# Performance work log

Measured on AMD Instinct MI355X. Metric: run time of the kernel, lower is better.

The kernel has to match this reference:

```python
import jax, jax.numpy as jnp
import numpy as np

# Mega (Flash-Quad) encoder layer: MultiHeadEMA + moving-average gated chunked attention + ScaleNorm
L, B, D = 2048, 16, 512        # seq_len, batch, embed_dim (fairseq L,B,D layout)
H, Z, NDIM = 1024, 128, 2      # hdim, zdim, EMA ndim
CHUNK = 128                    # Flash-Quad chunk size
MAXPOS = 1024                  # SimpleRelativePositionalBias max positions
EPS = 1e-6                     # ScaleNorm eps


def setup_inputs() -> dict:
    key = jax.random.key(0)
    ks = jax.random.split(key, 16)
    def nrm(k, shape, s=0.02):
        return jax.random.normal(k, shape, jnp.float32) * s
    return dict(
        x=jax.random.normal(ks[0], (L, B, D), jnp.float32),
        # MultiHeadEMA params (bidirectional -> kernel_dim = 2*D)
        ema_delta=nrm(ks[1], (2 * D, NDIM, 1), 1.0),
        ema_alpha=nrm(ks[2], (2 * D, NDIM, 1), 1.0),
        ema_beta=nrm(ks[3], (2 * D, NDIM, 1), 0.02),
        ema_gamma=nrm(ks[4], (2 * D, NDIM), 1.0),
        ema_omega=nrm(ks[5], (D,), 1.0),
        # projections
        Wv=nrm(ks[6], (D, H)), bv=jnp.zeros((H,), jnp.float32),
        Wmx=nrm(ks[7], (D, Z + H + 2 * D)), bmx=jnp.zeros((Z + H + 2 * D,), jnp.float32),
        Wh=nrm(ks[8], (H, D)), bh=jnp.zeros((D,), jnp.float32),
        # per-dim q/k affine (gamma/beta) on shared z
        qk_gamma=nrm(ks[9], (2, Z), 0.1) + 1.0,
        qk_beta=nrm(ks[10], (2, Z), 0.1),
        # simple relative positional bias over chunk length
        rel_pos_bias=nrm(ks[11], (2 * MAXPOS - 1,), 0.02),
        # ScaleNorm scalar
        norm_scalar=jnp.ones((), jnp.float32),
    )


def _ema(x, delta, alpha, beta, gamma, omega):
    """Bidirectional multi-dim damped EMA via FFT convolution. x: (L,B,D) -> (L,B,D)."""
    Lx, Bx, Dx = x.shape
    residual = x * omega
    xt = jnp.transpose(x, (1, 2, 0))                      # B,D,L
    p = jax.nn.sigmoid(delta)                             # 2D,n,1
    q = 1.0 - p * jax.nn.sigmoid(alpha)                   # 2D,n,1 in (0,1)
    vander = jnp.arange(Lx, dtype=jnp.float32)[None, None, :] * jnp.log(q)  # 2D,n,L
    kern = jnp.einsum('dnl,dn->dl', (p * beta) * jnp.exp(vander),
                      gamma * (1.0 / np.sqrt(NDIM)))      # 2D,L
    k1, k2 = kern[:Dx], kern[Dx:]
    # combined causal + anticausal kernel of length 2L-1, input left-padded by L-1
    kc = jnp.pad(k1, ((0, 0), (Lx - 1, 0))) + jnp.pad(k2[:, ::-1], ((0, 0), (0, Lx - 1)))
    xp = jnp.pad(xt, ((0, 0), (0, 0), (Lx - 1, 0)))
    n = 2 * (2 * Lx - 1)
    out = jnp.fft.irfft(jnp.fft.rfft(xp, n=n) * jnp.fft.rfft(kc, n=n), n=n)
    out = out[..., 2 * Lx - 2: 2 * Lx - 2 + Lx]           # B,D,L
    return jax.nn.silu(jnp.transpose(out, (2, 0, 1)) + residual)


def _forward(x, ema_delta, ema_alpha, ema_beta, ema_gamma, ema_omega,
             Wv, bv, Wmx, bmx, Wh, bh, qk_gamma, qk_beta, rel_pos_bias, norm_scalar):
    Lx, Bx, Dx = x.shape
    residual = x
    v = jax.nn.silu(x @ Wv + bv)                          # L,B,H
    mx = _ema(x, ema_delta, ema_alpha, ema_beta, ema_gamma, ema_omega)  # L,B,D
    base = mx @ Wmx + bmx                                 # L,B,D+Z+H+D
    u = jax.nn.sigmoid(base[..., :Dx])                    # update gate
    zr = jax.nn.silu(base[..., Dx:Dx + Z + H])
    hx = base[..., Dx + Z + H:]
    z, r = zr[..., :Z], zr[..., Z:]                       # shared z, reset gate r
    zqk = z[..., None, :] * qk_gamma + qk_beta            # L,B,2,Z
    nc = Lx // CHUNK
    q = jnp.transpose(zqk[..., 0, :], (1, 0, 2)).reshape(Bx, nc, CHUNK, Z)
    k = jnp.transpose(zqk[..., 1, :], (1, 0, 2)).reshape(Bx, nc, CHUNK, Z)
    vc = jnp.transpose(v, (1, 0, 2)).reshape(Bx, nc, CHUNK, H)
    # Toeplitz relative bias: bias[i,j] = rel_pos_bias[MAXPOS-1 + j - i]
    idx = (MAXPOS - 1) + jnp.arange(CHUNK)[None, :] - jnp.arange(CHUNK)[:, None]
    bias = rel_pos_bias[idx]                              # C,C
    qk = jnp.einsum('bnqz,bnkz->bnqk', q * (Z ** -0.5), k) + bias
    attn = jax.nn.softmax(qk, axis=-1)                    # B,nc,C,C
    h = jnp.einsum('bnqk,bnkh->bnqh', attn, vc).reshape(Bx, Lx, H)
    h = jnp.transpose(h, (1, 0, 2))                       # L,B,H
    h = jax.nn.silu(hx + (h * r) @ Wh + bh)               # L,B,D
    out = residual + u * (h - residual)                   # addcmul gated residual
    ms = jnp.mean(out * out, axis=-1, keepdims=True)      # ScaleNorm
    out = norm_scalar * out * jax.lax.rsqrt(ms + EPS)
    return out, attn


def reference(x, ema_delta, ema_alpha, ema_beta, ema_gamma, ema_omega,
              Wv, bv, Wmx, bmx, Wh, bh, qk_gamma, qk_beta, rel_pos_bias, norm_scalar):
    return _forward(x, ema_delta, ema_alpha, ema_beta, ema_gamma, ema_omega,
                    Wv, bv, Wmx, bmx, Wh, bh, qk_gamma, qk_beta, rel_pos_bias, norm_scalar)
```

## Files before the change

### kernel.cpp

```cpp
#include <hip/hip_runtime.h>
#include <math.h>

#define L_DIM 2048
#define B_DIM 16
#define D_DIM 512
#define H_DIM 1024
#define Z_DIM 128
#define NC    16
#define BASE_N 2176
#define ROWS  (L_DIM*B_DIM)
#define NSEG  32
#define SLEN  64
#define CHAINS 8192

typedef unsigned short bf16_t;
typedef __attribute__((ext_vector_type(8))) short short8;
typedef __attribute__((ext_vector_type(4))) float f32x4;

__device__ __forceinline__ float sigmoidf_(float x){ return 1.f/(1.f+__expf(-x)); }
__device__ __forceinline__ float siluf_(float x){ return x/(1.f+__expf(-x)); }
__device__ __forceinline__ float fbits(unsigned int b){ union{unsigned int i; float f;} c; c.i=b; return c.f; }
__device__ __forceinline__ unsigned short f2bf(float f){
  union{float f; unsigned int i;} c; c.f=f;
  unsigned int r = c.i + 0x7FFFu + ((c.i>>16)&1u);
  return (unsigned short)(r>>16);
}
__device__ __forceinline__ float bf2f(unsigned short u){ return fbits(((unsigned int)u)<<16); }

__device__ __forceinline__ void load8(const float* __restrict__ p, float* d){
  float4 a = *(const float4*)p; float4 b = *(const float4*)(p+4);
  d[0]=a.x; d[1]=a.y; d[2]=a.z; d[3]=a.w; d[4]=b.x; d[5]=b.y; d[6]=b.z; d[7]=b.w;
}
__device__ __forceinline__ void load8(const bf16_t* __restrict__ p, float* d){
  uint4 u = *(const uint4*)p;
  d[0]=fbits(u.x<<16); d[1]=fbits(u.x&0xFFFF0000u);
  d[2]=fbits(u.y<<16); d[3]=fbits(u.y&0xFFFF0000u);
  d[4]=fbits(u.z<<16); d[5]=fbits(u.z&0xFFFF0000u);
  d[6]=fbits(u.w<<16); d[7]=fbits(u.w&0xFFFF0000u);
}
__device__ __forceinline__ void store8bf(bf16_t* p, const float* v){
  uint4 s;
  s.x = (unsigned int)f2bf(v[0]) | ((unsigned int)f2bf(v[1])<<16);
  s.y = (unsigned int)f2bf(v[2]) | ((unsigned int)f2bf(v[3])<<16);
  s.z = (unsigned int)f2bf(v[4]) | ((unsigned int)f2bf(v[5])<<16);
  s.w = (unsigned int)f2bf(v[6]) | ((unsigned int)f2bf(v[7])<<16);
  *(uint4*)p = s;
}

__device__ __forceinline__ void glds16(const void* g, void* l) {
  __builtin_amdgcn_global_load_lds(
      (const __attribute__((address_space(1))) unsigned int*)g,
      (__attribute__((address_space(3))) unsigned int*)l, 16, 0, 0);
}

__global__ __launch_bounds__(256) void transpose_all_kernel(
    const float* __restrict__ Wv, const float* __restrict__ Wmx,
    const float* __restrict__ Wh, bf16_t* __restrict__ Wvt,
    bf16_t* __restrict__ Wmxt, bf16_t* __restrict__ Wht)
{
  __shared__ float t[32][33];
  int blk = blockIdx.x;
  const float* W; bf16_t* Wt; int K, N, bx, by;
  if (blk < 512)       { W=Wv;  Wt=Wvt;  K=512;  N=1024; bx=blk&31;  by=blk>>5; }
  else if (blk < 1600) { blk-=512;  W=Wmx; Wt=Wmxt; K=512;  N=2176; bx=blk%68; by=blk/68; }
  else                 { blk-=1600; W=Wh;  Wt=Wht;  K=1024; N=512;  bx=blk&15; by=blk>>4; }
  int lx = threadIdx.x & 31, ly = threadIdx.x >> 5;
  #pragma unroll
  for (int i = 0; i < 32; i += 8)
    t[ly+i][lx] = W[(size_t)(by*32+ly+i)*N + bx*32 + lx];
  __syncthreads();
  #pragma unroll
  for (int i = 0; i < 32; i += 8)
    Wt[(size_t)(bx*32+ly+i)*K + by*32 + lx] = f2bf(t[lx][ly+i]);
}

__global__ __launch_bounds__(256) void ema_carry_kernel(
    const float* __restrict__ x, const float* __restrict__ delta,
    const float* __restrict__ alpha, bf16_t* __restrict__ xb,
    float* __restrict__ carry)
{
  int idx = blockIdx.x*256 + threadIdx.x;
  int d = idx & 511, c = idx & 8191, s = idx >> 13;
  float qf0 = 1.f - sigmoidf_(delta[d*2+0])*sigmoidf_(alpha[d*2+0]);
  float qf1 = 1.f - sigmoidf_(delta[d*2+1])*sigmoidf_(alpha[d*2+1]);
  int dd = d + 512;
  float qb0 = 1.f - sigmoidf_(delta[dd*2+0])*sigmoidf_(alpha[dd*2+0]);
  float qb1 = 1.f - sigmoidf_(delta[dd*2+1])*sigmoidf_(alpha[dd*2+1]);
  size_t off = (size_t)s*SLEN*CHAINS + c;
  float xr[SLEN];
  float h0=0.f, h1=0.f;
  #pragma unroll
  for (int t = 0; t < SLEN; ++t) {
    size_t a = off + (size_t)t*CHAINS;
    float xv = x[a];
    unsigned short xv16 = f2bf(xv);
    xb[a] = xv16;
    xr[t] = bf2f(xv16);
    h0 = fmaf(qf0, h0, xv); h1 = fmaf(qf1, h1, xv);
  }
  float g0=0.f, g1=0.f;
  #pragma unroll
  for (int t = SLEN-1; t >= 0; --t) {
    float xv = xr[t];
    g0 = fmaf(qb0, g0, xv); g1 = fmaf(qb1, g1, xv);
  }
  carry[(size_t)s*CHAINS + c]              = h0;
  carry[(size_t)s*CHAINS + c + 262144]     = h1;
  carry[(size_t)s*CHAINS + c + 524288]     = g0;
  carry[(size_t)s*CHAINS + c + 786432]     = g1;
}

__global__ __launch_bounds__(256) void ema_combine_kernel(
    const float* __restrict__ delta, const float* __restrict__ alpha,
    float* __restrict__ carry)
{
  int c = blockIdx.x*256 + threadIdx.x;
  int d = c & 511;
  float qf0 = 1.f - sigmoidf_(delta[d*2+0])*sigmoidf_(alpha[d*2+0]);
  float qf1 = 1.f - sigmoidf_(delta[d*2+1])*sigmoidf_(alpha[d*2+1]);
  int dd = d + 512;
  float qb0 = 1.f - sigmoidf_(delta[dd*2+0])*sigmoidf_(alpha[dd*2+0]);
  float qb1 = 1.f - sigmoidf_(delta[dd*2+1])*sigmoidf_(alpha[dd*2+1]);
  float df0=qf0, df1=qf1, db0=qb0, db1=qb1;
  #pragma unroll
  for (int i = 0; i < 6; ++i) { df0*=df0; df1*=df1; db0*=db0; db1*=db1; }
  float h0=0.f, h1=0.f;
  for (int s = 0; s < NSEG; ++s) {
    size_t a = (size_t)s*CHAINS + c;
    float t0 = carry[a], t1 = carry[a+262144];
    carry[a] = h0; carry[a+262144] = h1;
    h0 = fmaf(df0, h0, t0); h1 = fmaf(df1, h1, t1);
  }
  float g0=0.f, g1=0.f;
  for (int s = NSEG-1; s >= 0; --s) {
    size_t a = (size_t)s*CHAINS + c;
    float t0 = carry[a+524288], t1 = carry[a+786432];
    carry[a+524288] = g0; carry[a+786432] = g1;
    g0 = fmaf(db0, g0, t0); g1 = fmaf(db1, g1, t1);
  }
}

__global__ __launch_bounds__(256) void ema_apply_kernel(
    const bf16_t* __restrict__ xb, const float* __restrict__ delta,
    const float* __restrict__ alpha, const float* __restrict__ beta,
    const float* __restrict__ gamma, const float* __restrict__ omega,
    const float* __restrict__ carry, bf16_t* __restrict__ mx)
{
  int idx = blockIdx.x*256 + threadIdx.x;
  int d = idx & 511, c = idx & 8191, s = idx >> 13;
  const float rs = 0.70710678118654752f;
  float pf0 = sigmoidf_(delta[d*2+0]), pf1 = sigmoidf_(delta[d*2+1]);
  float qf0 = 1.f - pf0*sigmoidf_(alpha[d*2+0]);
  float qf1 = 1.f - pf1*sigmoidf_(alpha[d*2+1]);
  float cf0 = pf0*beta[d*2+0]*gamma[d*2+0]*rs;
  float cf1 = pf1*beta[d*2+1]*gamma[d*2+1]*rs;
  int dd = d + 512;
  float pb0 = sigmoidf_(delta[dd*2+0]), pb1 = sigmoidf_(delta[dd*2+1]);
  float qb0 = 1.f - pb0*sigmoidf_(alpha[dd*2+0]);
  float qb1 = 1.f - pb1*sigmoidf_(alpha[dd*2+1]);
  float cb0 = pb0*beta[dd*2+0]*gamma[dd*2+0]*rs;
  float cb1 = pb1*beta[dd*2+1]*gamma[dd*2+1]*rs;
  float om = omega[d];
  size_t off = (size_t)s*SLEN*CHAINS + c;
  float h0 = carry[(size_t)s*CHAINS + c];
  float h1 = carry[(size_t)s*CHAINS + c + 262144];
  float yv[SLEN];
  #pragma unroll
  for (int t = 0; t < SLEN; ++t) {
    float xv = bf2f(xb[off + (size_t)t*CHAINS]);
    h0 = fmaf(qf0, h0, xv); h1 = fmaf(qf1, h1, xv);
    yv[t] = fmaf(cf0, h0, cf1*h1);
  }
  float g0 = carry[(size_t)s*CHAINS + c + 524288];
  float g1 = carry[(size_t)s*CHAINS + c + 786432];
  #pragma unroll
  for (int t = SLEN-1; t >= 0; --t) {
    size_t a = off + (size_t)t*CHAINS;
    float xv = bf2f(xb[a]);
    g0 = fmaf(qb0, g0, xv); g1 = fmaf(qb1, g1, xv);
    float sv = yv[t] + fmaf(cb0, g0, cb1*g1) + xv*om;
    mx[a] = f2bf(siluf_(sv));
  }
}

#define GEMM_SMEM                                                            \
  __shared__ __align__(16) char smem[24576];                                 \
  bf16_t* As = (bf16_t*)smem;                                    \
  bf16_t* Bs = (bf16_t*)(smem + 16384);                          \
  bf16_t* Cs = (bf16_t*)smem;

#define GEMM_PROLOG(Aptr, Bptr, Kdim)                                        \
  int tid = threadIdx.x;                                                     \
  int wave = tid >> 6, lane = tid & 63;                                      \
  int lrow = lane >> 3, lchunk = ((lane & 7) - lrow) & 7;                    \
  const bf16_t* Ag = (Aptr) + (size_t)(wave*32 + lrow)*(Kdim) + lchunk*8;    \
  const bf16_t* Bg = (Bptr) + (size_t)(wave*16 + lrow)*(Kdim) + lchunk*8;    \
  int wm = wave >> 1, wn = wave & 1;                                         \
  int fr = lane & 15, fq = lane >> 4;                                        \
  f32x4 acc[4][2];                                                           \
  _Pragma("unroll") for (int i = 0; i < 4; ++i)                              \
    _Pragma("unroll") for (int j = 0; j < 2; ++j)                            \
      acc[i][j] = (f32x4){0.f,0.f,0.f,0.f};

#define GEMM_KLOOP(Kdim)                                                     \
  for (int k0 = 0; k0 < (Kdim); k0 += 64) {                                  \
    __syncthreads();                                                         \
    _Pragma("unroll") for (int j = 0; j < 4; ++j)                            \
      glds16(Ag + (size_t)j*8*(Kdim) + k0, As + (wave*32 + j*8)*64);         \
    _Pragma("unroll") for (int j = 0; j < 2; ++j)                            \
      glds16(Bg + (size_t)j*8*(Kdim) + k0, Bs + (wave*16 + j*8)*64);         \
    __syncthreads();                                                         \
    _Pragma("unroll") for (int kk = 0; kk < 2; ++kk) {                       \
      short8 af[4], bfr[2];                                                  \
      _Pragma("unroll") for (int mi = 0; mi < 4; ++mi) {                     \
        int R = wm*64 + mi*16 + fr;                                          \
        af[mi] = *(const short8*)&As[R*64 + (((kk<<2)+fq+R)&7)*8];           \
      }                                                                      \
      _Pragma("unroll") for (int ni = 0; ni < 2; ++ni) {                     \
        int R = wn*32 + ni*16 + fr;                                          \
        bfr[ni] = *(const short8*)&Bs[R*64 + (((kk<<2)+fq+R)&7)*8];          \
      }                                                                      \
      _Pragma("unroll") for (int mi = 0; mi < 4; ++mi)                       \
        _Pragma("unroll") for (int ni = 0; ni < 2; ++ni)                     \
          acc[mi][ni] = __builtin_amdgcn_mfma_f32_16x16x32_bf16(             \
              af[mi], bfr[ni], acc[mi][ni], 0, 0, 0);                        \
    }                                                                        \
  }

__global__ __launch_bounds__(256, 6) void mfma_gemm_kernel(
    const bf16_t* __restrict__ A, const bf16_t* __restrict__ Bt,
    const float* __restrict__ bias, const bf16_t* __restrict__ Add, int addLd,
    bf16_t* __restrict__ C, int N, int K, int nT, int act)
{
  GEMM_SMEM
  int flat = blockIdx.x;
  int xcd = flat & 7, g = flat >> 3;
  int mT8 = (int)(gridDim.x / (unsigned)nT) >> 3;
  int mt = xcd*mT8 + g / nT;
  int nt = g % nT;
  int m0 = mt*128, n0 = nt*64;
  GEMM_PROLOG(A + (size_t)m0*K, Bt + (size_t)n0*K, K)
  GEMM_KLOOP(K)
  __syncthreads();
  #pragma unroll
  for (int ni = 0; ni < 2; ++ni) {
    int cl = wn*32 + ni*16 + fr;
    int gn = n0 + cl;
    float bv = bias[gn];
    #pragma unroll
    for (int mi = 0; mi < 4; ++mi) {
      #pragma unroll
      for (int r = 0; r < 4; ++r) {
        int ml = wm*64 + mi*16 + fq*4 + r;
        float val = acc[mi][ni][r] + bv;
        if (Add) val += bf2f(Add[(size_t)(m0+ml)*addLd + gn]);
        if (act == 1) val = siluf_(val);
        Cs[ml*72 + cl] = f2bf(val);
      }
    }
  }
  __syncthreads();
  int row = tid >> 1, c0 = (tid & 1)*32;
  #pragma unroll
  for (int q = 0; q < 4; ++q)
    *(uint4*)(C + (size_t)(m0+row)*N + n0 + c0 + q*8) =
        *(const uint4*)&Cs[row*72 + c0 + q*8];
}

__global__ __launch_bounds__(256, 6) void mfma_gemm_v_kernel(
    const bf16_t* __restrict__ A, const bf16_t* __restrict__ Bt,
    const float* __restrict__ bias, bf16_t* __restrict__ vt, int nT, int K)
{
  GEMM_SMEM
  int flat = blockIdx.x;
  int xcd = flat & 7, g = flat >> 3;
  int mT8 = (int)(gridDim.x / (unsigned)nT) >> 3;
  int mt = xcd*mT8 + g / nT;
  int nt = g % nT;
  int m0 = mt*128, n0 = nt*64;
  GEMM_PROLOG(A + (size_t)m0*K, Bt + (size_t)n0*K, K)
  GEMM_KLOOP(K)
  __syncthreads();
  #pragma unroll
  for (int ni = 0; ni < 2; ++ni) {
    int cl = wn*32 + ni*16 + fr;
    float bv = bias[n0 + cl];
    #pragma unroll
    for (int mi = 0; mi < 4; ++mi) {
      #pragma unroll
      for (int r = 0; r < 4; ++r) {
        int ml = wm*64 + mi*16 + fq*4 + r;
        Cs[ml*72 + cl] = f2bf(siluf_(acc[mi][ni][r] + bv));
      }
    }
  }
  __syncthreads();
  if (tid < 128) {
    int b = tid >> 3, h0l = (tid & 7)*8;
    int nchunk = mt >> 4, kbase = (mt & 15)*8;
    #pragma unroll
    for (int j = 0; j < 8; ++j) {
      int hl = h0l + j;
      uint4 s;
      s.x = (unsigned int)Cs[(0*16 + b)*72 + hl] |
            ((unsigned int)Cs[(1*16 + b)*72 + hl] << 16);
      s.y = (unsigned int)Cs[(2*16 + b)*72 + hl] |
            ((unsigned int)Cs[(3*16 + b)*72 + hl] << 16);
      s.z = (unsigned int)Cs[(4*16 + b)*72 + hl] |
            ((unsigned int)Cs[(5*16 + b)*72 + hl] << 16);
      s.w = (unsigned int)Cs[(6*16 + b)*72 + hl] |
            ((unsigned int)Cs[(7*16 + b)*72 + hl] << 16);
      *(uint4*)&vt[((size_t)(b*NC + nchunk)*H_DIM + n0 + hl)*128 + kbase] = s;
    }
  }
}

__global__ __launch_bounds__(256) void attn_scores_mfma_kernel(
    const bf16_t* __restrict__ base, const float* __restrict__ qkg,
    const float* __restrict__ qkb, const float* __restrict__ rpb,
    float* __restrict__ attn_out, bf16_t* __restrict__ p_bf)
{
  __shared__ bf16_t qs[128*136];
  __shared__ bf16_t ks[128*136];
  int blk = blockIdx.x;
  int b = blk >> 4, n = blk & 15;
  int tid = threadIdx.x;
  {
    int r = tid >> 1, z0 = (tid & 1)*64;
    size_t rowoff = ((size_t)((n*128 + r)*B_DIM + b))*BASE_N + 512 + z0;
    #pragma unroll
    for (int cchunk = 0; cchunk < 8; ++cchunk) {
      float t8[8], qv[8], kv[8];
      load8(base + rowoff + cchunk*8, t8);
      #pragma unroll
      for (int j = 0; j < 8; ++j) {
        int z = z0 + cchunk*8 + j;
        float zs = siluf_(t8[j]);
        qv[j] = fmaf(zs, qkg[z],     qkb[z]);
        kv[j] = fmaf(zs, qkg[128+z], qkb[128+z]);
      }
      store8bf(&qs[r*136 + z0 + cchunk*8], qv);
      store8bf(&ks[r*136 + z0 + cchunk*8], kv);
    }
  }
  __syncthreads();
  int wave = tid >> 6, lane = tid & 63;
  int fr = lane & 15, fq = lane >> 4;
  f32x4 acc[2][8];
  #pragma unroll
  for (int i = 0; i < 2; ++i)
    #pragma unroll
    for (int j = 0; j < 8; ++j)
      acc[i][j] = (f32x4){0.f,0.f,0.f,0.f};
  #pragma unroll
  for (int kk = 0; kk < 4; ++kk) {
    short8 af[2], bfr[8];
    #pragma unroll
    for (int mi = 0; mi < 2; ++mi)
      af[mi] = *(const short8*)&qs[(wave*32 + mi*16 + fr)*136 + kk*32 + fq*8];
    #pragma unroll
    for (int ni = 0; ni < 8; ++ni)
      bfr[ni] = *(const short8*)&ks[(ni*16 + fr)*136 + kk*32 + fq*8];
    #pragma unroll
    for (int mi = 0; mi < 2; ++mi)
      #pragma unroll
      for (int ni = 0; ni < 8; ++ni)
        acc[mi][ni] = __builtin_amdgcn_mfma_f32_16x16x32_bf16(
            af[mi], bfr[ni], acc[mi][ni], 0, 0, 0);
  }
  const float scale = 0.08838834764831845f;
  float mrow[2][4], srow[2][4];
  #pragma unroll
  for (int mi = 0; mi < 2; ++mi)
    #pragma unroll
    for (int r = 0; r < 4; ++r) mrow[mi][r] = -1e30f;
  #pragma unroll
  for (int mi = 0; mi < 2; ++mi)
    #pragma unroll
    for (int ni = 0; ni < 8; ++ni)
      #pragma unroll
      for (int r = 0; r < 4; ++r) {
        int i = wave*32 + mi*16 + fq*4 + r;
        int j = ni*16 + fr;
        float v = fmaf(acc[mi][ni][r], scale, rpb[1023 + j - i]);
        acc[mi][ni][r] = v;
        mrow[mi][r] = fmaxf(mrow[mi][r], v);
      }
  #pragma unroll
  for (int mi = 0; mi < 2; ++mi)
    #pragma unroll
    for (int r = 0; r < 4; ++r) {
      float m = mrow[mi][r];
      m = fmaxf(m, __shfl_xor(m, 1));
      m = fmaxf(m, __shfl_xor(m, 2));
      m = fmaxf(m, __shfl_xor(m, 4));
      m = fmaxf(m, __shfl_xor(m, 8));
      mrow[mi][r] = m;
      srow[mi][r] = 0.f;
    }
  #pragma unroll
  for (int mi = 0; mi < 2; ++mi)
    #pragma unroll
    for (int ni = 0; ni < 8; ++ni)
      #pragma unroll
      for (int r = 0; r < 4; ++r) {
        float e = __expf(acc[mi][ni][r] - mrow[mi][r]);
        acc[mi][ni][r] = e;
        srow[mi][r] += e;
      }
  #pragma unroll
  for (int mi = 0; mi < 2; ++mi)
    #pragma unroll
    for (int r = 0; r < 4; ++r) {
      float s = srow[mi][r];
      s += __shfl_xor(s, 1);
      s += __shfl_xor(s, 2);
      s += __shfl_xor(s, 4);
      s += __shfl_xor(s, 8);
      srow[mi][r] = 1.f/s;
    }
  #pragma unroll
  for (int mi = 0; mi < 2; ++mi)
    #pragma unroll
    for (int r = 0; r < 4; ++r) {
      int i = wave*32 + mi*16 + fq*4 + r;
      size_t o = ((size_t)blk*128 + i)*128;
      #pragma unroll
      for (int ni = 0; ni < 8; ++ni) {
        float val = acc[mi][ni][r]*srow[mi][r];
        attn_out[o + ni*16 + fr] = val;
        p_bf[o + ni*16 + fr] = f2bf(val);
      }
    }
}

__global__ __launch_bounds__(256, 6) void attn_pv_kernel(
    const bf16_t* __restrict__ p_bf, const bf16_t* __restrict__ vt,
    const bf16_t* __restrict__ base, bf16_t* __restrict__ hr)
{
  GEMM_SMEM
  int blk = blockIdx.x >> 4, ht = blockIdx.x & 15;
  int b = blk >> 4, n = blk & 15;
  const int K = 128;
  GEMM_PROLOG(p_bf + (size_t)blk*(128*128),
              vt + ((size_t)blk*H_DIM + ht*64)*128, K)
  GEMM_KLOOP(K)
  __syncthreads();
  #pragma unroll
  for (int ni = 0; ni < 2; ++ni) {
    int cl = wn*32 + ni*16 + fr;
    int hg = ht*64 + cl;
    #pragma unroll
    for (int mi = 0; mi < 4; ++mi) {
      #pragma unroll
      for (int r = 0; r < 4; ++r) {
        int ml = wm*64 + mi*16 + fq*4 + r;
        size_t rowg = (size_t)((n*128 + ml)*B_DIM + b);
        float rg = bf2f(base[rowg*BASE_N + 640 + hg]);
        Cs[ml*72 + cl] = f2bf(acc[mi][ni][r]*siluf_(rg));
      }
    }
  }
  __syncthreads();
  int row = tid >> 1, c0 = (tid & 1)*32;
  size_t rowg = (size_t)((n*128 + row)*B_DIM + b);
  #pragma unroll
  for (int q = 0; q < 4; ++q)
    *(uint4*)(hr + rowg*H_DIM + ht*64 + c0 + q*8) =
        *(const uint4*)&Cs[row*72 + c0 + q*8];
}

__global__ __launch_bounds__(256) void final_kernel(
    const float* __restrict__ x, const bf16_t* __restrict__ h2,
    const bf16_t* __restrict__ base, const float* __restrict__ ns,
    float* __restrict__ out)
{
  int row = blockIdx.x*4 + (threadIdx.x >> 6);
  int t = threadIdx.x & 63;
  size_t ro = (size_t)row*D_DIM + t*8;
  float xv[8]; load8(x + ro, xv);
  float hv[8]; load8(h2 + ro, hv);
  float uv[8]; load8(base + (size_t)row*BASE_N + t*8, uv);
  float o[8];
  float ss = 0.f;
  #pragma unroll
  for (int i = 0; i < 8; ++i) {
    float u = sigmoidf_(uv[i]);
    o[i] = xv[i] + u*(hv[i] - xv[i]);
    ss += o[i]*o[i];
  }
  #pragma unroll
  for (int m = 1; m < 64; m <<= 1) ss += __shfl_xor(ss, m);
  float inv = rsqrtf(ss*(1.f/(float)D_DIM) + 1e-6f) * ns[0];
  float4 r0, r1;
  r0.x = o[0]*inv; r0.y = o[1]*inv; r0.z = o[2]*inv; r0.w = o[3]*inv;
  r1.x = o[4]*inv; r1.y = o[5]*inv; r1.z = o[6]*inv; r1.w = o[7]*inv;
  *(float4*)(out + ro) = r0;
  *(float4*)(out + ro + 4) = r1;
}

extern "C" void kernel_launch(void* const* d_in, const int* in_sizes, int n_in,
                              void* d_out, int out_size, void* d_ws, size_t ws_size,
                              hipStream_t stream)
{
  const float* x     = (const float*)d_in[0];
  const float* delta = (const float*)d_in[1];
  const float* alpha = (const float*)d_in[2];
  const float* beta  = (const float*)d_in[3];
  const float* gamma = (const float*)d_in[4];
  const float* omega = (const float*)d_in[5];
  const float* Wv    = (const float*)d_in[6];
  const float* bv    = (const float*)d_in[7];
  const float* Wmx   = (const float*)d_in[8];
  const float* bmx   = (const float*)d_in[9];
  const float* Wh    = (const float*)d_in[10];
  const float* bh    = (const float*)d_in[11];
  const float* qkg   = (const float*)d_in[12];
  const float* qkb   = (const float*)d_in[13];
  const float* rpb   = (const float*)d_in[14];
  const float* ns    = (const float*)d_in[15];

  float* out  = (float*)d_out;
  float* attn = out + (size_t)ROWS*D_DIM;

  char* outb = (char*)d_out;
  bf16_t* x_bf  = (bf16_t*)outb;
  bf16_t* p_bf  = (bf16_t*)outb;
  bf16_t* Wv_t  = (bf16_t*)(outb + 33554432ull);
  bf16_t* Wmx_t = (bf16_t*)(outb + 34603008ull);
  bf16_t* Wh_t  = (bf16_t*)(outb + 36831232ull);

  const size_t WS_NEED = 310378496ull;
  if (ws_size < WS_NEED) return;
  char* wsb = (char*)d_ws;
  bf16_t* mx_bf   = (bf16_t*)(wsb);
  bf16_t* vt      = (bf16_t*)(wsb + 33554432ull);
  bf16_t* base_bf = (bf16_t*)(wsb + 100663296ull);
  bf16_t* hr_bf   = (bf16_t*)(wsb + 243269632ull);
  float*  carry   = (float*)(wsb + 100663296ull);
  bf16_t* h2_bf   = mx_bf;

  transpose_all_kernel<<<2112, 256, 0, stream>>>(Wv, Wmx, Wh, Wv_t, Wmx_t, Wh_t);
  ema_carry_kernel<<<1024, 256, 0, stream>>>(x, delta, alpha, x_bf, carry);
  ema_combine_kernel<<<32, 256, 0, stream>>>(delta, alpha, carry);
  ema_apply_kernel<<<1024, 256, 0, stream>>>(x_bf, delta, alpha, beta, gamma,
                                             omega, carry, mx_bf);
  mfma_gemm_v_kernel<<<4096, 256, 0, stream>>>(x_bf, Wv_t, bv, vt, 16, D_DIM);
  mfma_gemm_kernel<<<8704, 256, 0, stream>>>(
      mx_bf, Wmx_t, bmx, nullptr, 0, base_bf, BASE_N, D_DIM, 34, 0);
  attn_scores_mfma_kernel<<<B_DIM*NC, 256, 0, stream>>>(
      base_bf, qkg, qkb, rpb, attn, p_bf);
  attn_pv_kernel<<<4096, 256, 0, stream>>>(p_bf, vt, base_bf, hr_bf);
  mfma_gemm_kernel<<<2048, 256, 0, stream>>>(
      hr_bf, Wh_t, bh, base_bf + 1664, BASE_N, h2_bf, D_DIM, H_DIM, 8, 1);
  final_kernel<<<ROWS/4, 256, 0, stream>>>(x, h2_bf, base_bf, ns, out);
}
```

Before: 601.4 us.

## Fuse attention scores/softmax with PV matmul, keeping probabilities in shared memory

Merges the score/softmax kernel and the P·V kernel into one kernel per (batch, chunk) block. The bf16 probability tile stays in LDS instead of being written to and re-read from global memory, and the block loops over the 16 H-tiles of V with register prefetch. This removes a launch and the global round trip for P. In exchange the PV work runs on only 256 blocks instead of 4096, which lowers parallelism and occupancy, and the block uses more LDS.

```diff
diff --git a/kernel.cpp b/kernel.cpp
--- a/kernel.cpp
+++ b/kernel.cpp
@@ -315,13 +315,18 @@
   }
 }
 
-__global__ __launch_bounds__(256) void attn_scores_mfma_kernel(
+__global__ __launch_bounds__(256) void attn_fused_kernel(
     const bf16_t* __restrict__ base, const float* __restrict__ qkg,
     const float* __restrict__ qkb, const float* __restrict__ rpb,
-    float* __restrict__ attn_out, bf16_t* __restrict__ p_bf)
-{
-  __shared__ bf16_t qs[128*136];
-  __shared__ bf16_t ks[128*136];
+    float* __restrict__ attn_out, const bf16_t* __restrict__ vt,
+    bf16_t* __restrict__ hr)
+{
+  __shared__ __align__(16) char smem[70656];
+  bf16_t* qs = (bf16_t*)smem;
+  bf16_t* ks = (bf16_t*)(smem + 34816);
+  bf16_t* ps = qs;
+  bf16_t* Vs = ks;
+  bf16_t* Cs = (bf16_t*)(smem + 52224);
   int blk = blockIdx.x;
   int b = blk >> 4, n = blk & 15;
   int tid = threadIdx.x;
@@ -419,6 +424,7 @@
       s += __shfl_xor(s, 8);
       srow[mi][r] = 1.f/s;
     }
+  __syncthreads();
   #pragma unroll
   for (int mi = 0; mi < 2; ++mi)
     #pragma unroll
@@ -429,45 +435,77 @@
       for (int ni = 0; ni < 8; ++ni) {
         float val = acc[mi][ni][r]*srow[mi][r];
         attn_out[o + ni*16 + fr] = val;
-        p_bf[o + ni*16 + fr] = f2bf(val);
-      }
-    }
-}
-
-__global__ __launch_bounds__(256, 6) void attn_pv_kernel(
-    const bf16_t* __restrict__ p_bf, const bf16_t* __restrict__ vt,
-    const bf16_t* __restrict__ base, bf16_t* __restrict__ hr)
-{
-  GEMM_SMEM
-  int blk = blockIdx.x >> 4, ht = blockIdx.x & 15;
-  int b = blk >> 4, n = blk & 15;
-  const int K = 128;
-  GEMM_PROLOG(p_bf + (size_t)blk*(128*128),
-              vt + ((size_t)blk*H_DIM + ht*64)*128, K)
-  GEMM_KLOOP(K)
-  __syncthreads();
-  #pragma unroll
-  for (int ni = 0; ni < 2; ++ni) {
-    int cl = wn*32 + ni*16 + fr;
-    int hg = ht*64 + cl;
-    #pragma unroll
-    for (int mi = 0; mi < 4; ++mi) {
-      #pragma unroll
-      for (int r = 0; r < 4; ++r) {
-        int ml = wm*64 + mi*16 + fq*4 + r;
-        size_t rowg = (size_t)((n*128 + ml)*B_DIM + b);
-        float rg = bf2f(base[rowg*BASE_N + 640 + hg]);
-        Cs[ml*72 + cl] = f2bf(acc[mi][ni][r]*siluf_(rg));
-      }
-    }
-  }
-  __syncthreads();
-  int row = tid >> 1, c0 = (tid & 1)*32;
-  size_t rowg = (size_t)((n*128 + row)*B_DIM + b);
-  #pragma unroll
-  for (int q = 0; q < 4; ++q)
-    *(uint4*)(hr + rowg*H_DIM + ht*64 + c0 + q*8) =
-        *(const uint4*)&Cs[row*72 + c0 + q*8];
+        ps[i*136 + ni*16 + fr] = f2bf(val);
+      }
+    }
+  int wm = wave >> 1, wn = wave & 1;
+  const bf16_t* vbase = vt + (size_t)blk*H_DIM*128;
+  uint4 vbuf[4];
+  {
+    const uint4* src = (const uint4*)vbase;
+    #pragma unroll
+    for (int it = 0; it < 4; ++it) vbuf[it] = src[it*256 + tid];
+  }
+  for (int ht = 0; ht < 16; ++ht) {
+    #pragma unroll
+    for (int it = 0; it < 4; ++it) {
+      int e = (it*256 + tid)*8;
+      int row = e >> 7, col = e & 127;
+      *(uint4*)&Vs[row*136 + col] = vbuf[it];
+    }
+    __syncthreads();
+    if (ht < 15) {
+      const uint4* src = (const uint4*)(vbase + (size_t)(ht+1)*64*128);
+      #pragma unroll
+      for (int it = 0; it < 4; ++it) vbuf[it] = src[it*256 + tid];
+    }
+    f32x4 acc2[4][2];
+    #pragma unroll
+    for (int i = 0; i < 4; ++i)
+      #pragma unroll
+      for (int j = 0; j < 2; ++j)
+        acc2[i][j] = (f32x4){0.f,0.f,0.f,0.f};
+    #pragma unroll
+    for (int kk = 0; kk < 4; ++kk) {
+      short8 af[4], bfr[2];
+      #pragma unroll
+      for (int mi = 0; mi < 4; ++mi)
+        af[mi] = *(const short8*)&ps[(wm*64 + mi*16 + fr)*136 + kk*32 + fq*8];
+      #pragma unroll
+      for (int ni = 0; ni < 2; ++ni)
+        bfr[ni] = *(const short8*)&Vs[(wn*32 + ni*16 + fr)*136 + kk*32 + fq*8];
+      #pragma unroll
+      for (int mi = 0; mi < 4; ++mi)
+        #pragma unroll
+        for (int ni = 0; ni < 2; ++ni)
+          acc2[mi][ni] = __builtin_amdgcn_mfma_f32_16x16x32_bf16(
+              af[mi], bfr[ni], acc2[mi][ni], 0, 0, 0);
+    }
+    #pragma unroll
+    for (int ni = 0; ni < 2; ++ni) {
+      int cl = wn*32 + ni*16 + fr;
+      int hg = ht*64 + cl;
+      #pragma unroll
+      for (int mi = 0; mi < 4; ++mi) {
+        #pragma unroll
+        for (int r = 0; r < 4; ++r) {
+          int ml = wm*64 + mi*16 + fq*4 + r;
+          size_t rowg = (size_t)((n*128 + ml)*B_DIM + b);
+          float rg = bf2f(base[rowg*BASE_N + 640 + hg]);
+          Cs[ml*72 + cl] = f2bf(acc2[mi][ni][r]*siluf_(rg));
+        }
+      }
+    }
+    __syncthreads();
+    {
+      int row = tid >> 1, c0 = (tid & 1)*32;
+      size_t rowg = (size_t)((n*128 + row)*B_DIM + b);
+      #pragma unroll
+      for (int q = 0; q < 4; ++q)
+        *(uint4*)(hr + rowg*H_DIM + ht*64 + c0 + q*8) =
+            *(const uint4*)&Cs[row*72 + c0 + q*8];
+    }
+  }
 }
 
 __global__ __launch_bounds__(256) void final_kernel(
@@ -525,7 +563,6 @@
 
   char* outb = (char*)d_out;
   bf16_t* x_bf  = (bf16_t*)outb;
-  bf16_t* p_bf  = (bf16_t*)outb;
   bf16_t* Wv_t  = (bf16_t*)(outb + 33554432ull);
   bf16_t* Wmx_t = (bf16_t*)(outb + 34603008ull);
   bf16_t* Wh_t  = (bf16_t*)(outb + 36831232ull);
@@ -548,9 +585,8 @@
   mfma_gemm_v_kernel<<<4096, 256, 0, stream>>>(x_bf, Wv_t, bv, vt, 16, D_DIM);
   mfma_gemm_kernel<<<8704, 256, 0, stream>>>(
       mx_bf, Wmx_t, bmx, nullptr, 0, base_bf, BASE_N, D_DIM, 34, 0);
-  attn_scores_mfma_kernel<<<B_DIM*NC, 256, 0, stream>>>(
-      base_bf, qkg, qkb, rpb, attn, p_bf);
-  attn_pv_kernel<<<4096, 256, 0, stream>>>(p_bf, vt, base_bf, hr_bf);
+  attn_fused_kernel<<<B_DIM*NC, 256, 0, stream>>>(
+      base_bf, qkg, qkb, rpb, attn, vt, hr_bf);
   mfma_gemm_kernel<<<2048, 256, 0, stream>>>(
       hr_bf, Wh_t, bh, base_bf + 1664, BASE_N, h2_bf, D_DIM, H_DIM, 8, 1);
   final_kernel<<<ROWS/4, 256, 0, stream>>>(x, h2_bf, base_bf, ns, out);
```

Result: slower. 636.0 us (+5.7%).
